# Optimization experiments

Hardware: AMD Instinct MI355X
Metric: run time of the kernel (lower is better)

The kernel has to match this reference:

```python
import jax, jax.numpy as jnp
import numpy as np

N_NODES = 100000
N_EDGES = 3200000
D_IN = 256
D_OUT = 256


def setup_inputs() -> dict:
    key = jax.random.key(0)
    k1, k2, k3, k4, k5 = jax.random.split(key, 5)
    features = jax.random.normal(k1, (N_NODES, D_IN), dtype=jnp.float32)
    # xavier_uniform init for the weight
    limit = np.sqrt(6.0 / (D_IN + D_OUT)).astype(np.float32)
    weight = jax.random.uniform(k2, (D_IN, D_OUT), minval=-limit, maxval=limit, dtype=jnp.float32)
    adj_row = jax.random.randint(k3, (N_EDGES,), 0, N_NODES, dtype=jnp.int64)
    adj_col = jax.random.randint(k4, (N_EDGES,), 0, N_NODES, dtype=jnp.int64)
    adj_val = jax.random.uniform(k5, (N_EDGES,), dtype=jnp.float32)
    return {"features": features, "weight": weight, "adj_row": adj_row,
            "adj_col": adj_col, "adj_val": adj_val}


def reference(features, weight, adj_row, adj_col, adj_val):
    # support = features @ W   (dense GEMM)
    support = features @ weight                      # [N, D_OUT]
    # spmm: out[i] = sum_e val[e] * support[col[e]] for edges with row[e] == i
    gathered = adj_val[:, None] * support[adj_col]   # [E, D_OUT]
    out = jax.ops.segment_sum(gathered, adj_row, num_segments=features.shape[0])
    return jax.nn.relu(out)
```

## Files before the change

kernel.cpp:

```cpp
#include <hip/hip_runtime.h>
#include <hip/hip_bf16.h>

#define N_NODES 100000
#define N_EDGES 3200000
#define NBUCK   391

typedef short v8s __attribute__((ext_vector_type(8)));
typedef float v4f __attribute__((ext_vector_type(4)));

__device__ __forceinline__ unsigned short f2b(float x) {
    __hip_bfloat16 h = __float2bfloat16(x);
    return *reinterpret_cast<unsigned short*>(&h);
}
__device__ __forceinline__ float b2f(unsigned short u) {
    return __uint_as_float(((unsigned int)u) << 16);
}

__device__ __forceinline__ void gld16(const void* g, void* l) {
    __builtin_amdgcn_global_load_lds(
        (const __attribute__((address_space(1))) void*)g,
        (__attribute__((address_space(3))) void*)l, 16, 0, 0);
}

__global__ void transpose_b(const float* __restrict__ B, unsigned short* __restrict__ BT) {
    int n = blockIdx.x;
    int k = threadIdx.x;
    BT[n * 256 + k] = f2b(B[k * 256 + n]);
}

__global__ __launch_bounds__(512)
void gemm_dma(const float* __restrict__ A, const unsigned short* __restrict__ BT,
              unsigned short* __restrict__ C) {
    __shared__ __align__(16) float          sA[128 * 64];
    __shared__ __align__(16) unsigned short sB[256 * 64];

    const int tid  = threadIdx.x;
    const int wave = tid >> 6;
    const int lane = tid & 63;
    const int quad = lane >> 4;
    const int l16  = lane & 15;
    const int row0 = blockIdx.x * 128;

    v4f acc[16];
#pragma unroll
    for (int t = 0; t < 16; t++) acc[t] = (v4f){0.f, 0.f, 0.f, 0.f};

    const int ml = wave * 16 + l16;

    for (int ks = 0; ks < 4; ks++) {
        const int kbase = ks * 64;
#pragma unroll
        for (int i = 0; i < 4; i++) {
            int s = i * 512 + tid;
            int m = s >> 4;
            int c = (s & 15) ^ (m & 15);
            int row = row0 + m;
            if (row >= N_NODES) row = row0;
            gld16(A + (size_t)row * 256 + kbase + c * 4, (char*)sA + (size_t)s * 16);
        }
#pragma unroll
        for (int i = 0; i < 4; i++) {
            int s = i * 512 + tid;
            int n = s >> 3;
            int c = (s & 7) ^ (n & 7);
            gld16(BT + (size_t)n * 256 + kbase + c * 8, (char*)sB + (size_t)s * 16);
        }
        __syncthreads();

#pragma unroll
        for (int sub = 0; sub < 2; sub++) {
            int ca  = sub * 8 + 2 * quad;
            int pa0 = ml * 16 + (ca ^ (ml & 15));
            int pa1 = ml * 16 + ((ca + 1) ^ (ml & 15));
            v4f lo = *(const v4f*)&sA[pa0 * 4];
            v4f hi = *(const v4f*)&sA[pa1 * 4];
            v8s af;
            af[0] = (short)f2b(lo[0]); af[1] = (short)f2b(lo[1]);
            af[2] = (short)f2b(lo[2]); af[3] = (short)f2b(lo[3]);
            af[4] = (short)f2b(hi[0]); af[5] = (short)f2b(hi[1]);
            af[6] = (short)f2b(hi[2]); af[7] = (short)f2b(hi[3]);
            int cb = sub * 4 + quad;
#pragma unroll
            for (int t = 0; t < 16; t++) {
                int n  = t * 16 + l16;
                int pb = n * 8 + (cb ^ (n & 7));
                v8s bf = *(const v8s*)&sB[pb * 8];
                acc[t] = __builtin_amdgcn_mfma_f32_16x16x32_bf16(af, bf, acc[t], 0, 0, 0);
            }
        }
        __syncthreads();
    }

    const int grow_base = row0 + wave * 16 + quad * 4;
#pragma unroll
    for (int t = 0; t < 16; t++) {
#pragma unroll
        for (int r = 0; r < 4; r++) {
            int grow = grow_base + r;
            if (grow < N_NODES)
                C[(size_t)grow * 256 + t * 16 + l16] = f2b(acc[t][r]);
        }
    }
}

__global__ __launch_bounds__(256)
void bhist_kernel(const int* __restrict__ row, int* __restrict__ ghist) {
    __shared__ int h[NBUCK];
    const int tid = threadIdx.x;
    for (int i = tid; i < NBUCK; i += 256) h[i] = 0;
    __syncthreads();
    const int e0 = blockIdx.x * 4096;
#pragma unroll
    for (int j = 0; j < 16; j++) {
        int e = e0 + j * 256 + tid;
        if (e < N_EDGES) atomicAdd(&h[row[e] >> 8], 1);
    }
    __syncthreads();
    for (int i = tid; i < NBUCK; i += 256)
        if (h[i]) atomicAdd(&ghist[i], h[i]);
}

__global__ void bscan_kernel(const int* __restrict__ ghist, int* __restrict__ bbase,
                             int* __restrict__ gcur) {
    __shared__ int s[512];
    const int tid = threadIdx.x;
    int x = (tid < NBUCK) ? ghist[tid] : 0;
    s[tid] = x;
    __syncthreads();
    for (int off = 1; off < 512; off <<= 1) {
        int v = (tid >= off) ? s[tid - off] : 0;
        __syncthreads();
        s[tid] += v;
        __syncthreads();
    }
    if (tid < NBUCK) {
        int b = s[tid] - x;
        bbase[tid] = b;
        gcur[tid]  = b;
    }
}

__global__ __launch_bounds__(512)
void bin2_kernel(const int* __restrict__ row, const int* __restrict__ col,
                 const float* __restrict__ val, int* __restrict__ gcur,
                 int2* __restrict__ bucket) {
    __shared__ int  cnt[512];
    __shared__ int  ls[512];
    __shared__ int  gb[512];
    __shared__ int  lcur[512];
    __shared__ __align__(16) int2 stage[4096];
    __shared__ int  gdst[4096];

    const int tid = threadIdx.x;
    const int e0  = blockIdx.x * 4096;

    int r[8], c[8];
    float v[8];
#pragma unroll
    for (int j = 0; j < 8; j++) {
        int e = e0 + j * 512 + tid;
        if (e < N_EDGES) { r[j] = row[e]; c[j] = col[e]; v[j] = val[e]; }
        else r[j] = -1;
    }

    cnt[tid] = 0;
    __syncthreads();
#pragma unroll
    for (int j = 0; j < 8; j++)
        if (r[j] >= 0) atomicAdd(&cnt[r[j] >> 8], 1);
    __syncthreads();

    int x = cnt[tid];
    int gbase = 0;
    if (x) gbase = atomicAdd(&gcur[tid], x);
    gb[tid] = gbase;

    lcur[tid] = x;
    __syncthreads();
    for (int off = 1; off < 512; off <<= 1) {
        int t = (tid >= off) ? lcur[tid - off] : 0;
        __syncthreads();
        lcur[tid] += t;
        __syncthreads();
    }
    int excl = lcur[tid] - x;
    __syncthreads();
    ls[tid]   = excl;
    lcur[tid] = excl;
    __syncthreads();

#pragma unroll
    for (int j = 0; j < 8; j++) {
        if (r[j] >= 0) {
            int b = r[j] >> 8;
            int q = atomicAdd(&lcur[b], 1);
            stage[q] = make_int2(((r[j] & 255) << 20) | c[j], __float_as_int(v[j]));
            gdst[q]  = gb[b] + (q - ls[b]);
        }
    }
    __syncthreads();

    int tot = N_EDGES - e0;
    if (tot > 4096) tot = 4096;
    for (int i = tid; i < tot; i += 512)
        bucket[gdst[i]] = stage[i];
}

__global__ __launch_bounds__(512)
void csort_kernel(const int2* __restrict__ bucket, const int* __restrict__ bbase,
                  const int* __restrict__ gcur, unsigned int* __restrict__ csr,
                  int* __restrict__ offs, int* __restrict__ counts) {
    __shared__ int h[256];
    __shared__ int s[512];
    __shared__ int cur[256];
    const int tid  = threadIdx.x;
    const int b    = blockIdx.x;
    const int base = bbase[b];
    const int end  = gcur[b];

    if (tid < 256) h[tid] = 0;
    __syncthreads();
    for (int i = base + tid; i < end; i += 512)
        atomicAdd(&h[bucket[i].x >> 20], 1);
    __syncthreads();

    int x = (tid < 256) ? h[tid] : 0;
    s[tid] = x;
    __syncthreads();
    for (int off = 1; off < 512; off <<= 1) {
        int v2 = (tid >= off) ? s[tid - off] : 0;
        __syncthreads();
        s[tid] += v2;
        __syncthreads();
    }
    if (tid < 256) {
        int ro = s[tid] - x;
        int grow = b * 256 + tid;
        if (grow < N_NODES) {
            offs[grow]   = base + ro;
            counts[grow] = x;
        }
        cur[tid] = base + ro;
    }
    __syncthreads();

    for (int i = base + tid; i < end; i += 512) {
        int2 w = bucket[i];
        int rl = w.x >> 20;
        int p  = atomicAdd(&cur[rl], 1);
        unsigned int vb = (((unsigned int)w.y + 0x8000u) >> 16) & 0x7FFFu;
        csr[p] = (vb << 17) | (unsigned int)(w.x & 0x1FFFF);
    }
}

__global__ __launch_bounds__(256)
void spmm_kernel(const unsigned short* __restrict__ sup,
                 const int* __restrict__ offs, const int* __restrict__ counts,
                 const unsigned int* __restrict__ csr, float* __restrict__ out) {
    const int wave = threadIdx.x >> 6;
    const int lane = threadIdx.x & 63;
    const int row  = blockIdx.x * 4 + wave;
    if (row >= N_NODES) return;

    const int start = offs[row];
    const int deg   = counts[row];

    float a0 = 0.f, a1 = 0.f, a2 = 0.f, a3 = 0.f;

    for (int base = 0; base < deg; base += 64) {
        int nb = deg - base;
        if (nb > 64) nb = 64;
        int c = 0;
        float v = 0.f;
        if (lane < nb) {
            unsigned int w = csr[start + base + lane];
            c = (int)(w & 0x1FFFFu);
            v = __uint_as_float((w >> 17) << 16);
        }
        int j = 0;
        for (; j + 8 <= nb; j += 8) {
            int   cc[8];
            float vv[8];
#pragma unroll
            for (int u = 0; u < 8; u++) { cc[u] = __shfl(c, j + u); vv[u] = __shfl(v, j + u); }
            ushort4 h[8];
#pragma unroll
            for (int u = 0; u < 8; u++)
                h[u] = *(const ushort4*)(sup + (size_t)cc[u] * 256 + lane * 4);
#pragma unroll
            for (int u = 0; u < 8; u++) {
                a0 += vv[u] * b2f(h[u].x); a1 += vv[u] * b2f(h[u].y);
                a2 += vv[u] * b2f(h[u].z); a3 += vv[u] * b2f(h[u].w);
            }
        }
        for (; j + 4 <= nb; j += 4) {
            int   c0 = __shfl(c, j),     c1 = __shfl(c, j + 1);
            int   c2 = __shfl(c, j + 2), c3 = __shfl(c, j + 3);
            float v0 = __shfl(v, j),     v1 = __shfl(v, j + 1);
            float v2 = __shfl(v, j + 2), v3 = __shfl(v, j + 3);
            ushort4 h0 = *(const ushort4*)(sup + (size_t)c0 * 256 + lane * 4);
            ushort4 h1 = *(const ushort4*)(sup + (size_t)c1 * 256 + lane * 4);
            ushort4 h2 = *(const ushort4*)(sup + (size_t)c2 * 256 + lane * 4);
            ushort4 h3 = *(const ushort4*)(sup + (size_t)c3 * 256 + lane * 4);
            a0 += v0 * b2f(h0.x); a1 += v0 * b2f(h0.y);
            a2 += v0 * b2f(h0.z); a3 += v0 * b2f(h0.w);
            a0 += v1 * b2f(h1.x); a1 += v1 * b2f(h1.y);
            a2 += v1 * b2f(h1.z); a3 += v1 * b2f(h1.w);
            a0 += v2 * b2f(h2.x); a1 += v2 * b2f(h2.y);
            a2 += v2 * b2f(h2.z); a3 += v2 * b2f(h2.w);
            a0 += v3 * b2f(h3.x); a1 += v3 * b2f(h3.y);
            a2 += v3 * b2f(h3.z); a3 += v3 * b2f(h3.w);
        }
        for (; j < nb; j++) {
            int   cj = __shfl(c, j);
            float vj = __shfl(v, j);
            ushort4 hh = *(const ushort4*)(sup + (size_t)cj * 256 + lane * 4);
            a0 += vj * b2f(hh.x); a1 += vj * b2f(hh.y);
            a2 += vj * b2f(hh.z); a3 += vj * b2f(hh.w);
        }
    }

    float4 o;
    o.x = a0 > 0.f ? a0 : 0.f;
    o.y = a1 > 0.f ? a1 : 0.f;
    o.z = a2 > 0.f ? a2 : 0.f;
    o.w = a3 > 0.f ? a3 : 0.f;
    *(float4*)(out + (size_t)row * 256 + lane * 4) = o;
}

extern "C" void kernel_launch(void* const* d_in, const int* in_sizes, int n_in,
                              void* d_out, int out_size, void* d_ws, size_t ws_size,
                              hipStream_t stream) {
    const float* features = (const float*)d_in[0];
    const float* weight   = (const float*)d_in[1];
    const int*   adj_row  = (const int*)d_in[2];
    const int*   adj_col  = (const int*)d_in[3];
    const float* adj_val  = (const float*)d_in[4];
    float* out = (float*)d_out;

    char* ws = (char*)d_ws;
    size_t off = 0;
    auto alloc = [&](size_t bytes) -> char* {
        char* p = ws + off;
        off = (off + bytes + 255) & ~(size_t)255;
        return p;
    };
    unsigned short* sup     = (unsigned short*)alloc((size_t)N_NODES * 256 * 2);
    unsigned short* BT      = (unsigned short*)alloc(256 * 256 * 2);
    int*            counts  = (int*)alloc((size_t)N_NODES * 4);
    int*            offsets = (int*)alloc((size_t)N_NODES * 4);
    int*            ghist   = (int*)alloc(512 * 4);
    int*            bbase   = (int*)alloc(512 * 4);
    int*            gcur    = (int*)alloc(512 * 4);
    int2*           bucket  = (int2*)alloc((size_t)N_EDGES * 8);
    unsigned int*   csr     = (unsigned int*)alloc((size_t)N_EDGES * 4);

    hipMemsetAsync(ghist, 0, 512 * 4, stream);

    transpose_b<<<256, 256, 0, stream>>>(weight, BT);
    gemm_dma<<<782, 512, 0, stream>>>(features, BT, sup);
    bhist_kernel<<<782, 256, 0, stream>>>(adj_row, ghist);
    bscan_kernel<<<1, 512, 0, stream>>>(ghist, bbase, gcur);
    bin2_kernel<<<782, 512, 0, stream>>>(adj_row, adj_col, adj_val, gcur, bucket);
    csort_kernel<<<NBUCK, 512, 0, stream>>>(bucket, bbase, gcur, csr, offsets, counts);
    spmm_kernel<<<25000, 256, 0, stream>>>(sup, offsets, counts, csr, out);
}
```

Before: 511.0 us.

## Split SpMM into column halves, shrink bucket payload, use wave-shuffle scans

Bucket entries are split into a 4-byte key array and a 2-byte bf16 value array, with the value converted to bf16 in the binning pass. This cuts the scatter and sort traffic from 8 to 6 bytes per edge. The block-level LDS scans in binning and counting sort are replaced with wave shuffle scans, and the counting sort runs 1024 threads per block. SpMM now runs as two launches, each covering 128 output columns. Four edges are processed at once with 16-byte loads per lane, followed by a cross-quarter shuffle reduction. The half-width gather is meant to keep a smaller working set of the support matrix in cache, but it reads the CSR twice and adds a launch.

```diff
diff --git a/kernel.cpp b/kernel.cpp
--- a/kernel.cpp
+++ b/kernel.cpp
@@ -7,6 +7,7 @@
 
 typedef short v8s __attribute__((ext_vector_type(8)));
 typedef float v4f __attribute__((ext_vector_type(4)));
+typedef unsigned short v8u __attribute__((ext_vector_type(8)));
 
 __device__ __forceinline__ unsigned short f2b(float x) {
     __hip_bfloat16 h = __float2bfloat16(x);
@@ -141,26 +142,30 @@
 }
 
 __global__ __launch_bounds__(512)
-void bin2_kernel(const int* __restrict__ row, const int* __restrict__ col,
+void bin3_kernel(const int* __restrict__ row, const int* __restrict__ col,
                  const float* __restrict__ val, int* __restrict__ gcur,
-                 int2* __restrict__ bucket) {
-    __shared__ int  cnt[512];
-    __shared__ int  ls[512];
-    __shared__ int  gb[512];
-    __shared__ int  lcur[512];
-    __shared__ __align__(16) int2 stage[4096];
-    __shared__ int  gdst[4096];
+                 unsigned int* __restrict__ bucketK, unsigned short* __restrict__ bucketV) {
+    __shared__ int cnt[512];
+    __shared__ int ls[512];
+    __shared__ int gb[512];
+    __shared__ int lcur[512];
+    __shared__ int wsum[8];
+    __shared__ __align__(16) unsigned int   skey[4096];
+    __shared__ unsigned short sval[4096];
+    __shared__ unsigned short sbid[4096];
 
     const int tid = threadIdx.x;
     const int e0  = blockIdx.x * 4096;
 
     int r[8], c[8];
-    float v[8];
+    unsigned short v[8];
 #pragma unroll
     for (int j = 0; j < 8; j++) {
         int e = e0 + j * 512 + tid;
-        if (e < N_EDGES) { r[j] = row[e]; c[j] = col[e]; v[j] = val[e]; }
-        else r[j] = -1;
+        if (e < N_EDGES) {
+            r[j] = row[e]; c[j] = col[e];
+            v[j] = (unsigned short)((((unsigned int)__float_as_int(val[e]) + 0x8000u) >> 16) & 0x7FFFu);
+        } else r[j] = -1;
     }
 
     cnt[tid] = 0;
@@ -171,20 +176,21 @@
     __syncthreads();
 
     int x = cnt[tid];
-    int gbase = 0;
-    if (x) gbase = atomicAdd(&gcur[tid], x);
-    gb[tid] = gbase;
-
-    lcur[tid] = x;
-    __syncthreads();
-    for (int off = 1; off < 512; off <<= 1) {
-        int t = (tid >= off) ? lcur[tid - off] : 0;
-        __syncthreads();
-        lcur[tid] += t;
-        __syncthreads();
-    }
-    int excl = lcur[tid] - x;
-    __syncthreads();
+    gb[tid] = x ? atomicAdd(&gcur[tid], x) : 0;
+
+    const int lane = tid & 63, w = tid >> 6;
+    int inc = x;
+#pragma unroll
+    for (int d = 1; d < 64; d <<= 1) {
+        int t = __shfl_up(inc, d);
+        if (lane >= d) inc += t;
+    }
+    if (lane == 63) wsum[w] = inc;
+    __syncthreads();
+    int pre = 0;
+#pragma unroll
+    for (int k = 0; k < 8; k++) pre += (k < w) ? wsum[k] : 0;
+    int excl = pre + inc - x;
     ls[tid]   = excl;
     lcur[tid] = excl;
     __syncthreads();
@@ -194,25 +200,32 @@
         if (r[j] >= 0) {
             int b = r[j] >> 8;
             int q = atomicAdd(&lcur[b], 1);
-            stage[q] = make_int2(((r[j] & 255) << 20) | c[j], __float_as_int(v[j]));
-            gdst[q]  = gb[b] + (q - ls[b]);
+            skey[q] = ((unsigned int)(r[j] & 255) << 17) | (unsigned int)c[j];
+            sval[q] = v[j];
+            sbid[q] = (unsigned short)b;
         }
     }
     __syncthreads();
 
     int tot = N_EDGES - e0;
     if (tot > 4096) tot = 4096;
-    for (int i = tid; i < tot; i += 512)
-        bucket[gdst[i]] = stage[i];
-}
-
-__global__ __launch_bounds__(512)
-void csort_kernel(const int2* __restrict__ bucket, const int* __restrict__ bbase,
-                  const int* __restrict__ gcur, unsigned int* __restrict__ csr,
-                  int* __restrict__ offs, int* __restrict__ counts) {
+    for (int i = tid; i < tot; i += 512) {
+        int b   = sbid[i];
+        int dst = gb[b] + (i - ls[b]);
+        bucketK[dst] = skey[i];
+        bucketV[dst] = sval[i];
+    }
+}
+
+__global__ __launch_bounds__(1024)
+void csort3_kernel(const unsigned int* __restrict__ bucketK,
+                   const unsigned short* __restrict__ bucketV,
+                   const int* __restrict__ bbase, const int* __restrict__ gcur,
+                   unsigned int* __restrict__ csr,
+                   int* __restrict__ offs, int* __restrict__ counts) {
     __shared__ int h[256];
-    __shared__ int s[512];
     __shared__ int cur[256];
+    __shared__ int wsum4[4];
     const int tid  = threadIdx.x;
     const int b    = blockIdx.x;
     const int base = bbase[b];
@@ -220,112 +233,125 @@
 
     if (tid < 256) h[tid] = 0;
     __syncthreads();
-    for (int i = base + tid; i < end; i += 512)
-        atomicAdd(&h[bucket[i].x >> 20], 1);
-    __syncthreads();
-
-    int x = (tid < 256) ? h[tid] : 0;
-    s[tid] = x;
-    __syncthreads();
-    for (int off = 1; off < 512; off <<= 1) {
-        int v2 = (tid >= off) ? s[tid - off] : 0;
-        __syncthreads();
-        s[tid] += v2;
-        __syncthreads();
-    }
+    for (int i = base + tid; i < end; i += 1024)
+        atomicAdd(&h[bucketK[i] >> 17], 1);
+    __syncthreads();
+
+    int x = 0, inc = 0;
     if (tid < 256) {
-        int ro = s[tid] - x;
+        x = h[tid];
+        inc = x;
+        const int lane = tid & 63;
+#pragma unroll
+        for (int d = 1; d < 64; d <<= 1) {
+            int t = __shfl_up(inc, d);
+            if (lane >= d) inc += t;
+        }
+        if (lane == 63) wsum4[tid >> 6] = inc;
+    }
+    __syncthreads();
+    if (tid < 256) {
+        int pre = 0;
+#pragma unroll
+        for (int k = 0; k < 4; k++) pre += (k < (tid >> 6)) ? wsum4[k] : 0;
+        int excl = pre + inc - x;
         int grow = b * 256 + tid;
         if (grow < N_NODES) {
-            offs[grow]   = base + ro;
+            offs[grow]   = base + excl;
             counts[grow] = x;
         }
-        cur[tid] = base + ro;
-    }
-    __syncthreads();
-
-    for (int i = base + tid; i < end; i += 512) {
-        int2 w = bucket[i];
-        int rl = w.x >> 20;
+        cur[tid] = base + excl;
+    }
+    __syncthreads();
+
+    for (int i = base + tid; i < end; i += 1024) {
+        unsigned int k   = bucketK[i];
+        unsigned int v15 = bucketV[i];
+        int rl = (int)(k >> 17);
         int p  = atomicAdd(&cur[rl], 1);
-        unsigned int vb = (((unsigned int)w.y + 0x8000u) >> 16) & 0x7FFFu;
-        csr[p] = (vb << 17) | (unsigned int)(w.x & 0x1FFFF);
+        csr[p] = (v15 << 17) | (k & 0x1FFFFu);
     }
 }
 
 __global__ __launch_bounds__(256)
-void spmm_kernel(const unsigned short* __restrict__ sup,
-                 const int* __restrict__ offs, const int* __restrict__ counts,
-                 const unsigned int* __restrict__ csr, float* __restrict__ out) {
+void spmm_half(const unsigned short* __restrict__ sup,
+               const int* __restrict__ offs, const int* __restrict__ counts,
+               const unsigned int* __restrict__ csr, float* __restrict__ out,
+               const int cbase) {
     const int wave = threadIdx.x >> 6;
     const int lane = threadIdx.x & 63;
     const int row  = blockIdx.x * 4 + wave;
     if (row >= N_NODES) return;
 
+    const int q   = lane >> 4;
+    const int c16 = lane & 15;
+    const unsigned short* supc = sup + cbase + c16 * 8;
+
     const int start = offs[row];
     const int deg   = counts[row];
 
-    float a0 = 0.f, a1 = 0.f, a2 = 0.f, a3 = 0.f;
-
-    for (int base = 0; base < deg; base += 64) {
-        int nb = deg - base;
+    float a[8];
+#pragma unroll
+    for (int k = 0; k < 8; k++) a[k] = 0.f;
+
+    for (int base2 = 0; base2 < deg; base2 += 64) {
+        int nb = deg - base2;
         if (nb > 64) nb = 64;
         int c = 0;
         float v = 0.f;
         if (lane < nb) {
-            unsigned int w = csr[start + base + lane];
+            unsigned int w = csr[start + base2 + lane];
             c = (int)(w & 0x1FFFFu);
             v = __uint_as_float((w >> 17) << 16);
         }
-        int j = 0;
-        for (; j + 8 <= nb; j += 8) {
-            int   cc[8];
-            float vv[8];
-#pragma unroll
-            for (int u = 0; u < 8; u++) { cc[u] = __shfl(c, j + u); vv[u] = __shfl(v, j + u); }
-            ushort4 h[8];
-#pragma unroll
-            for (int u = 0; u < 8; u++)
-                h[u] = *(const ushort4*)(sup + (size_t)cc[u] * 256 + lane * 4);
-#pragma unroll
-            for (int u = 0; u < 8; u++) {
-                a0 += vv[u] * b2f(h[u].x); a1 += vv[u] * b2f(h[u].y);
-                a2 += vv[u] * b2f(h[u].z); a3 += vv[u] * b2f(h[u].w);
+        int ng = (nb + 3) >> 2;
+        int g = 0;
+        for (; g + 4 <= ng; g += 4) {
+            int cc[4]; float vv[4];
+#pragma unroll
+            for (int u = 0; u < 4; u++) {
+                int idx = (g + u) * 4 + q;
+                cc[u] = __shfl(c, idx);
+                vv[u] = __shfl(v, idx);
             }
-        }
-        for (; j + 4 <= nb; j += 4) {
-            int   c0 = __shfl(c, j),     c1 = __shfl(c, j + 1);
-            int   c2 = __shfl(c, j + 2), c3 = __shfl(c, j + 3);
-            float v0 = __shfl(v, j),     v1 = __shfl(v, j + 1);
-            float v2 = __shfl(v, j + 2), v3 = __shfl(v, j + 3);
-            ushort4 h0 = *(const ushort4*)(sup + (size_t)c0 * 256 + lane * 4);
-            ushort4 h1 = *(const ushort4*)(sup + (size_t)c1 * 256 + lane * 4);
-            ushort4 h2 = *(const ushort4*)(sup + (size_t)c2 * 256 + lane * 4);
-            ushort4 h3 = *(const ushort4*)(sup + (size_t)c3 * 256 + lane * 4);
-            a0 += v0 * b2f(h0.x); a1 += v0 * b2f(h0.y);
-            a2 += v0 * b2f(h0.z); a3 += v0 * b2f(h0.w);
-            a0 += v1 * b2f(h1.x); a1 += v1 * b2f(h1.y);
-            a2 += v1 * b2f(h1.z); a3 += v1 * b2f(h1.w);
-            a0 += v2 * b2f(h2.x); a1 += v2 * b2f(h2.y);
-            a2 += v2 * b2f(h2.z); a3 += v2 * b2f(h2.w);
-            a0 += v3 * b2f(h3.x); a1 += v3 * b2f(h3.y);
-            a2 += v3 * b2f(h3.z); a3 += v3 * b2f(h3.w);
-        }
-        for (; j < nb; j++) {
-            int   cj = __shfl(c, j);
-            float vj = __shfl(v, j);
-            ushort4 hh = *(const ushort4*)(sup + (size_t)cj * 256 + lane * 4);
-            a0 += vj * b2f(hh.x); a1 += vj * b2f(hh.y);
-            a2 += vj * b2f(hh.z); a3 += vj * b2f(hh.w);
-        }
-    }
-
-    float4 o;
-    o.x = a0 > 0.f ? a0 : 0.f;
-    o.y = a1 > 0.f ? a1 : 0.f;
-    o.z = a2 > 0.f ? a2 : 0.f;
-    o.w = a3 > 0.f ? a3 : 0.f;
-    *(float4*)(out + (size_t)row * 256 + lane * 4) = o;
+            v8u h[4];
+#pragma unroll
+            for (int u = 0; u < 4; u++)
+                h[u] = *(const v8u*)(supc + (size_t)cc[u] * 256);
+#pragma unroll
+            for (int u = 0; u < 4; u++) {
+#pragma unroll
+                for (int k = 0; k < 8; k++)
+                    a[k] += vv[u] * b2f(h[u][k]);
+            }
+        }
+        for (; g < ng; g++) {
+            int idx = g * 4 + q;
+            int   cc = __shfl(c, idx);
+            float vv = __shfl(v, idx);
+            v8u h = *(const v8u*)(supc + (size_t)cc * 256);
+#pragma unroll
+            for (int k = 0; k < 8; k++)
+                a[k] += vv * b2f(h[k]);
+        }
+    }
+
+#pragma unroll
+    for (int k = 0; k < 8; k++) {
+        a[k] += __shfl_xor(a[k], 16);
+        a[k] += __shfl_xor(a[k], 32);
+    }
+
+    if (lane < 32) {
+        int q2 = lane >> 4;
+        int cl = lane & 15;
+        float4 o;
+        o.x = a[q2 * 4 + 0] > 0.f ? a[q2 * 4 + 0] : 0.f;
+        o.y = a[q2 * 4 + 1] > 0.f ? a[q2 * 4 + 1] : 0.f;
+        o.z = a[q2 * 4 + 2] > 0.f ? a[q2 * 4 + 2] : 0.f;
+        o.w = a[q2 * 4 + 3] > 0.f ? a[q2 * 4 + 3] : 0.f;
+        *(float4*)(out + (size_t)row * 256 + cbase + cl * 8 + q2 * 4) = o;
+    }
 }
 
 extern "C" void kernel_launch(void* const* d_in, const int* in_sizes, int n_in,
@@ -352,7 +378,8 @@
     int*            ghist   = (int*)alloc(512 * 4);
     int*            bbase   = (int*)alloc(512 * 4);
     int*            gcur    = (int*)alloc(512 * 4);
-    int2*           bucket  = (int2*)alloc((size_t)N_EDGES * 8);
+    unsigned int*   bucketK = (unsigned int*)alloc((size_t)N_EDGES * 4);
+    unsigned short* bucketV = (unsigned short*)alloc((size_t)N_EDGES * 2);
     unsigned int*   csr     = (unsigned int*)alloc((size_t)N_EDGES * 4);
 
     hipMemsetAsync(ghist, 0, 512 * 4, stream);
@@ -361,7 +388,8 @@
     gemm_dma<<<782, 512, 0, stream>>>(features, BT, sup);
     bhist_kernel<<<782, 256, 0, stream>>>(adj_row, ghist);
     bscan_kernel<<<1, 512, 0, stream>>>(ghist, bbase, gcur);
-    bin2_kernel<<<782, 512, 0, stream>>>(adj_row, adj_col, adj_val, gcur, bucket);
-    csort_kernel<<<NBUCK, 512, 0, stream>>>(bucket, bbase, gcur, csr, offsets, counts);
-    spmm_kernel<<<25000, 256, 0, stream>>>(sup, offsets, counts, csr, out);
-}
+    bin3_kernel<<<782, 512, 0, stream>>>(adj_row, adj_col, adj_val, gcur, bucketK, bucketV);
+    csort3_kernel<<<NBUCK, 1024, 0, stream>>>(bucketK, bucketV, bbase, gcur, csr, offsets, counts);
+    spmm_half<<<25000, 256, 0, stream>>>(sup, offsets, counts, csr, out, 0);
+    spmm_half<<<25000, 256, 0, stream>>>(sup, offsets, counts, csr, out, 128);
+}
```

Result: no change. 502.6 us (-1.6%).
